# Kernel optimization log

Hardware: AMD Instinct MI355X
Metric: run time of the kernel (lower is better)

## Reference

```python
import jax, jax.numpy as jnp
import numpy as np

N_NODES = 100000
N_EDGES = 1600000
IN_CH = 64
HID = 64
OUT_CH = 16
T = 1.0


def _gat_layer(x, edge_index, W, b, t):
    # x: [N, d_in]; W: [d_out, d_in] (torch Linear weight layout); b: [d_out]
    N = x.shape[0]
    loop = jnp.arange(N, dtype=edge_index.dtype)
    src = jnp.concatenate([edge_index[0], loop])  # add self loops
    dst = jnp.concatenate([edge_index[1], loop])
    h = x @ W.T  # [N, d_out]
    x_i = h[dst]  # target node features per edge
    x_j = h[src]  # source node features per edge
    alpha = jnp.sum(x_i * x_j, axis=-1)  # [E']
    alpha = jnp.where(alpha > 0, jnp.asarray(t, h.dtype), jnp.asarray(-t, h.dtype))
    # segment softmax grouped by edge_index[0] (source), faithful to original
    m = jax.ops.segment_max(alpha, src, num_segments=N)
    e = jnp.exp(alpha - m[src])
    s = jax.ops.segment_sum(e, src, num_segments=N)
    w = e / s[src]
    msg = x_j * w[:, None]
    out = jax.ops.segment_sum(msg, dst, num_segments=N)  # scatter-add to target
    return out + b


def setup_inputs() -> dict:
    key = jax.random.key(0)
    k1, k2, k3, k4 = jax.random.split(key, 4)
    x = jax.random.normal(k1, (N_NODES, IN_CH), dtype=jnp.float32)
    edge_index = jax.random.randint(k2, (2, N_EDGES), 0, N_NODES, dtype=jnp.int64)
    # xavier-uniform-ish linear weights, torch layout [out, in]
    lim1 = float(np.sqrt(6.0 / (IN_CH + HID)))
    W1 = jax.random.uniform(k3, (HID, IN_CH), jnp.float32, -lim1, lim1)
    lim2 = float(np.sqrt(6.0 / (HID + OUT_CH)))
    W2 = jax.random.uniform(k4, (OUT_CH, HID), jnp.float32, -lim2, lim2)
    b1 = jnp.zeros((HID,), jnp.float32)
    b2 = jnp.zeros((OUT_CH,), jnp.float32)
    return {"x": x, "edge_index": edge_index, "W1": W1, "b1": b1, "W2": W2, "b2": b2}


def reference(x, edge_index, W1, b1, W2, b2):
    h = _gat_layer(x, edge_index, W1, b1, T)
    h = jax.nn.relu(h)
    h = _gat_layer(h, edge_index, W2, b2, T)
    return jax.nn.log_softmax(h, axis=1)
```

## Files before the change

kernel.cpp:

```cpp
#include <hip/hip_runtime.h>

#define EXPC 0.13533528323661270f
#define REP 8
#define CHUNK 16384

__global__ void zero_i32(int* __restrict__ p, int n) {
  int i = blockIdx.x * blockDim.x + threadIdx.x;
  if (i < n) p[i] = 0;
}

template <bool RELU_IN>
__global__ void __launch_bounds__(256, 1)
gemm64_k(const float* __restrict__ x, const float* __restrict__ W,
         float* __restrict__ h, int N) {
  __shared__ float xs[64][68];
  __shared__ float wt[64][68];
  const int t = threadIdx.x;
  const int r0 = blockIdx.x * 64;
  for (int i = t; i < 4096; i += 256) {
    int c = i >> 6, k = i & 63;
    wt[k][c] = W[i];
  }
  for (int s = t; s < 1024; s += 256) {
    int r = s >> 4, c4 = (s & 15) << 2;
    float4 v = make_float4(0.f, 0.f, 0.f, 0.f);
    if (r0 + r < N) {
      v = *(const float4*)(x + (size_t)(r0 + r) * 64 + c4);
      if (RELU_IN) {
        v.x = fmaxf(v.x, 0.f); v.y = fmaxf(v.y, 0.f);
        v.z = fmaxf(v.z, 0.f); v.w = fmaxf(v.w, 0.f);
      }
    }
    *(float4*)(&xs[r][c4]) = v;
  }
  __syncthreads();
  const int ty = t >> 4, tx = t & 15;
  float acc[4][4] = {};
  for (int kk = 0; kk < 64; kk += 4) {
    float4 a[4], w[4];
#pragma unroll
    for (int i = 0; i < 4; i++) a[i] = *(const float4*)(&xs[4 * ty + i][kk]);
#pragma unroll
    for (int m = 0; m < 4; m++) w[m] = *(const float4*)(&wt[kk + m][4 * tx]);
#pragma unroll
    for (int i = 0; i < 4; i++) {
      acc[i][0] = fmaf(a[i].x, w[0].x, fmaf(a[i].y, w[1].x,
                  fmaf(a[i].z, w[2].x, fmaf(a[i].w, w[3].x, acc[i][0]))));
      acc[i][1] = fmaf(a[i].x, w[0].y, fmaf(a[i].y, w[1].y,
                  fmaf(a[i].z, w[2].y, fmaf(a[i].w, w[3].y, acc[i][1]))));
      acc[i][2] = fmaf(a[i].x, w[0].z, fmaf(a[i].y, w[1].z,
                  fmaf(a[i].z, w[2].z, fmaf(a[i].w, w[3].z, acc[i][2]))));
      acc[i][3] = fmaf(a[i].x, w[0].w, fmaf(a[i].y, w[1].w,
                  fmaf(a[i].z, w[2].w, fmaf(a[i].w, w[3].w, acc[i][3]))));
    }
  }
#pragma unroll
  for (int i = 0; i < 4; i++) {
    int row = r0 + 4 * ty + i;
    if (row < N)
      *(float4*)(h + (size_t)row * 64 + 4 * tx) =
          make_float4(acc[i][0], acc[i][1], acc[i][2], acc[i][3]);
  }
}

__global__ void passA_k(const int* __restrict__ ei, int* __restrict__ chd,
                        int* __restrict__ chs, int E, int Et) {
  __shared__ int ld[512], ls[512];
  int t = threadIdx.x;
  for (int i = t; i < 512; i += 256) { ld[i] = 0; ls[i] = 0; }
  __syncthreads();
  int base = blockIdx.x * CHUNK;
  int end = base + CHUNK; if (end > Et) end = Et;
  for (int e = base + t; e < end; e += 256) {
    int s, d;
    if (e < E) { s = ei[e]; d = ei[E + e]; } else { s = e - E; d = s; }
    atomicAdd(&ld[d >> 8], 1);
    atomicAdd(&ls[s >> 8], 1);
  }
  __syncthreads();
  for (int i = t; i < 512; i += 256) {
    if (ld[i]) atomicAdd(chd + i, ld[i]);
    if (ls[i]) atomicAdd(chs + i, ls[i]);
  }
}

__global__ void scan2_k(const int* __restrict__ chd, const int* __restrict__ chs,
                        int* __restrict__ cbd, int* __restrict__ cbs,
                        int* __restrict__ cud, int* __restrict__ cus, int NB) {
  __shared__ int l[512];
  int t = threadIdx.x;
  for (int pass = 0; pass < 2; ++pass) {
    const int* src = pass ? chs : chd;
    int* db = pass ? cbs : cbd;
    int* dc = pass ? cus : cud;
    int v = (t < NB) ? src[t] : 0;
    l[t] = v;
    __syncthreads();
    for (int o = 1; o < 512; o <<= 1) {
      int a = (t >= o) ? l[t - o] : 0;
      __syncthreads();
      l[t] += a;
      __syncthreads();
    }
    if (t < NB) { int e = l[t] - v; db[t] = e; dc[t] = e; }
    __syncthreads();
  }
}

__global__ void passB_k(const int* __restrict__ ei, int* __restrict__ cud,
                        int* __restrict__ cus, int* __restrict__ part_dst,
                        unsigned char* __restrict__ part_src, int E, int Et) {
  __shared__ int cntd[512], cnts[512], based[512], bases[512];
  int t = threadIdx.x;
  for (int i = t; i < 512; i += 256) { cntd[i] = 0; cnts[i] = 0; }
  __syncthreads();
  int base = blockIdx.x * CHUNK;
  int end = base + CHUNK; if (end > Et) end = Et;
  for (int e = base + t; e < end; e += 256) {
    int s, d;
    if (e < E) { s = ei[e]; d = ei[E + e]; } else { s = e - E; d = s; }
    atomicAdd(&cntd[d >> 8], 1);
    atomicAdd(&cnts[s >> 8], 1);
  }
  __syncthreads();
  for (int i = t; i < 512; i += 256) {
    based[i] = cntd[i] ? atomicAdd(cud + i, cntd[i]) : 0;
    bases[i] = cnts[i] ? atomicAdd(cus + i, cnts[i]) : 0;
    cntd[i] = 0; cnts[i] = 0;
  }
  __syncthreads();
  for (int e = base + t; e < end; e += 256) {
    int s, d;
    if (e < E) { s = ei[e]; d = ei[E + e]; } else { s = e - E; d = s; }
    int bd = d >> 8, bs = s >> 8;
    int rd = atomicAdd(&cntd[bd], 1);
    int rs = atomicAdd(&cnts[bs], 1);
    part_dst[based[bd] + rd] = s | ((d & 255) << 17);
    part_src[bases[bs] + rs] = (unsigned char)(s & 255);
  }
}

__global__ void passC_k(const int* __restrict__ part_dst, const int* __restrict__ cbd,
                        const int* __restrict__ chd, int* __restrict__ csr_src,
                        int* __restrict__ in_deg, int* __restrict__ off, int N) {
  __shared__ int hist[256], loff[256], rank[256];
  int b = blockIdx.x, t = threadIdx.x;
  int segbase = cbd[b], segcnt = chd[b];
  hist[t] = 0; rank[t] = 0;
  __syncthreads();
  for (int i = t; i < segcnt; i += 256)
    atomicAdd(&hist[part_dst[segbase + i] >> 17], 1);
  __syncthreads();
  int x = hist[t];
  loff[t] = x;
  __syncthreads();
  for (int o = 1; o < 256; o <<= 1) {
    int a = (t >= o) ? loff[t - o] : 0;
    __syncthreads();
    loff[t] += a;
    __syncthreads();
  }
  int excl = loff[t] - x;
  int node = (b << 8) + t;
  if (node < N) { in_deg[node] = x; off[node] = segbase + excl; }
  __syncthreads();
  loff[t] = excl;
  __syncthreads();
  for (int i = t; i < segcnt; i += 256) {
    int rec = part_dst[segbase + i];
    int dl = rec >> 17;
    int r = atomicAdd(&rank[dl], 1);
    csr_src[segbase + loff[dl] + r] = rec & 0x1FFFF;
  }
}

__global__ void passCs_k(const unsigned char* __restrict__ part_src,
                         const int* __restrict__ cbs, const int* __restrict__ chs,
                         int* __restrict__ deg, int N) {
  __shared__ int hist[256];
  int b = blockIdx.x, t = threadIdx.x;
  int segbase = cbs[b], segcnt = chs[b];
  hist[t] = 0;
  __syncthreads();
  for (int i = t; i < segcnt; i += 256)
    atomicAdd(&hist[part_src[segbase + i]], 1);
  __syncthreads();
  int node = (b << 8) + t;
  if (node < N) deg[node] = hist[t];
}

template <int D>
__global__ void __launch_bounds__(256, 1)
alpha_csr_k(const int* __restrict__ csr_src, const int* __restrict__ off,
            const int* __restrict__ indeg, const float* __restrict__ h,
            unsigned char* __restrict__ flagb, int* __restrict__ pos_rep, int N) {
  const int G = D / 4;
  int t = blockIdx.x * 256 + threadIdx.x;
  int node = t / G;
  int c = t & (G - 1);
  if (node >= N) return;
  int* pos = pos_rep + (blockIdx.x & (REP - 1)) * N;
  const float4 hd = *(const float4*)(h + (size_t)node * D + c * 4);
  int j = off[node];
  int je = j + indeg[node];
  for (; j + 8 <= je; j += 8) {
    int s[8];
    float4 a[8];
#pragma unroll
    for (int u = 0; u < 8; u++) s[u] = csr_src[j + u];
#pragma unroll
    for (int u = 0; u < 8; u++) a[u] = *(const float4*)(h + (size_t)s[u] * D + c * 4);
    float p[8];
#pragma unroll
    for (int u = 0; u < 8; u++)
      p[u] = fmaf(a[u].x, hd.x, fmaf(a[u].y, hd.y, fmaf(a[u].z, hd.z, a[u].w * hd.w)));
#pragma unroll
    for (int o = G / 2; o > 0; o >>= 1) {
#pragma unroll
      for (int u = 0; u < 8; u++) p[u] += __shfl_xor(p[u], o);
    }
    if (c == 0) {
#pragma unroll
      for (int u = 0; u < 8; u++) {
        bool z = p[u] > 0.f;
        flagb[j + u] = (unsigned char)z;
        if (z) atomicAdd(pos + s[u], 1);
      }
    }
  }
  for (; j < je; ++j) {
    int s = csr_src[j];
    float4 hs = *(const float4*)(h + (size_t)s * D + c * 4);
    float p = fmaf(hs.x, hd.x, fmaf(hs.y, hd.y, fmaf(hs.z, hd.z, hs.w * hd.w)));
#pragma unroll
    for (int o = G / 2; o > 0; o >>= 1) p += __shfl_xor(p, o);
    if (c == 0) {
      bool pz = p > 0.f;
      flagb[j] = (unsigned char)pz;
      if (pz) atomicAdd(pos + s, 1);
    }
  }
}

template <int D>
__global__ void denom_scale_k(const int* __restrict__ pos_rep, const int* __restrict__ deg,
                              float* __restrict__ h, int N) {
  const int G = D / 4;
  int t = blockIdx.x * 256 + threadIdx.x;
  int node = t / G;
  int c = t & (G - 1);
  if (node >= N) return;
  float dinv = 0.f;
  if (c == 0) {
    int p = 0;
#pragma unroll
    for (int r = 0; r < REP; r++) p += pos_rep[r * N + node];
    int dg = deg[node];
    dinv = (p > 0) ? 1.f / ((float)p + (float)(dg - p) * EXPC)
                   : 1.f / (EXPC * (float)dg);
  }
  dinv = __shfl(dinv, 0, G);
  float4* hp = (float4*)(h + (size_t)node * D + c * 4);
  float4 v = *hp;
  v.x *= dinv; v.y *= dinv; v.z *= dinv; v.w *= dinv;
  *hp = v;
}

__global__ void __launch_bounds__(256, 1)
gather1_g16_k(const int* __restrict__ csr_src, const int* __restrict__ off,
              const int* __restrict__ indeg, const unsigned char* __restrict__ flagb,
              const float* __restrict__ h, const float* __restrict__ b1,
              const float* __restrict__ W2, float* __restrict__ h2, int N) {
  __shared__ float wt2[16][68];
  const int t = threadIdx.x;
  for (int i = t; i < 1024; i += 256) wt2[i >> 6][i & 63] = W2[i];
  __syncthreads();
  int g = blockIdx.x * 256 + t;
  int node = g >> 4;
  int c = g & 15;
  if (node >= N) return;
  float4 acc = *(const float4*)(b1 + c * 4);
  int j = off[node];
  int je = j + indeg[node];
  for (; j + 8 <= je; j += 8) {
    int s[8];
    float w[8];
    float4 v[8];
#pragma unroll
    for (int u = 0; u < 8; u++) s[u] = csr_src[j + u];
#pragma unroll
    for (int u = 0; u < 8; u++) w[u] = flagb[j + u] ? 1.f : EXPC;
#pragma unroll
    for (int u = 0; u < 8; u++) v[u] = *(const float4*)(h + (size_t)s[u] * 64 + c * 4);
#pragma unroll
    for (int u = 0; u < 8; u++) {
      acc.x = fmaf(w[u], v[u].x, acc.x);
      acc.y = fmaf(w[u], v[u].y, acc.y);
      acc.z = fmaf(w[u], v[u].z, acc.z);
      acc.w = fmaf(w[u], v[u].w, acc.w);
    }
  }
  for (; j < je; ++j) {
    int s = csr_src[j];
    float w = flagb[j] ? 1.f : EXPC;
    float4 hv = *(const float4*)(h + (size_t)s * 64 + c * 4);
    acc.x = fmaf(w, hv.x, acc.x);
    acc.y = fmaf(w, hv.y, acc.y);
    acc.z = fmaf(w, hv.z, acc.z);
    acc.w = fmaf(w, hv.w, acc.w);
  }
  acc.x = fmaxf(acc.x, 0.f); acc.y = fmaxf(acc.y, 0.f);
  acc.z = fmaxf(acc.z, 0.f); acc.w = fmaxf(acc.w, 0.f);
  int lanebase = (threadIdx.x & 63) & 48;
  float o = 0.f;
#pragma unroll
  for (int s16 = 0; s16 < 16; s16++) {
    int src = lanebase + s16;
    float cx = __shfl(acc.x, src);
    float cy = __shfl(acc.y, src);
    float cz = __shfl(acc.z, src);
    float cw = __shfl(acc.w, src);
    float4 wv = *(const float4*)(&wt2[c][4 * s16]);
    o = fmaf(cx, wv.x, fmaf(cy, wv.y, fmaf(cz, wv.z, fmaf(cw, wv.w, o))));
  }
  h2[(size_t)node * 16 + c] = o;
}

__global__ void __launch_bounds__(256, 1)
gather2_k(const int* __restrict__ csr_src, const int* __restrict__ off,
          const int* __restrict__ indeg, const unsigned char* __restrict__ flagb,
          const float* __restrict__ h, const float* __restrict__ b2,
          float* __restrict__ outp, int N) {
  int t = blockIdx.x * 256 + threadIdx.x;
  int node = t >> 2;
  int c = t & 3;
  if (node >= N) return;
  float4 acc = *(const float4*)(b2 + c * 4);
  int j = off[node];
  int je = j + indeg[node];
  for (; j + 8 <= je; j += 8) {
    int s[8];
    float w[8];
    float4 v[8];
#pragma unroll
    for (int u = 0; u < 8; u++) s[u] = csr_src[j + u];
#pragma unroll
    for (int u = 0; u < 8; u++) w[u] = flagb[j + u] ? 1.f : EXPC;
#pragma unroll
    for (int u = 0; u < 8; u++) v[u] = *(const float4*)(h + (size_t)s[u] * 16 + c * 4);
#pragma unroll
    for (int u = 0; u < 8; u++) {
      acc.x = fmaf(w[u], v[u].x, acc.x);
      acc.y = fmaf(w[u], v[u].y, acc.y);
      acc.z = fmaf(w[u], v[u].z, acc.z);
      acc.w = fmaf(w[u], v[u].w, acc.w);
    }
  }
  for (; j < je; ++j) {
    int s = csr_src[j];
    float w = flagb[j] ? 1.f : EXPC;
    float4 hv = *(const float4*)(h + (size_t)s * 16 + c * 4);
    acc.x = fmaf(w, hv.x, acc.x);
    acc.y = fmaf(w, hv.y, acc.y);
    acc.z = fmaf(w, hv.z, acc.z);
    acc.w = fmaf(w, hv.w, acc.w);
  }
  float m = fmaxf(fmaxf(acc.x, acc.y), fmaxf(acc.z, acc.w));
  m = fmaxf(m, __shfl_xor(m, 1));
  m = fmaxf(m, __shfl_xor(m, 2));
  float s = expf(acc.x - m) + expf(acc.y - m) + expf(acc.z - m) + expf(acc.w - m);
  s += __shfl_xor(s, 1);
  s += __shfl_xor(s, 2);
  float lse = m + logf(s);
  acc.x -= lse; acc.y -= lse; acc.z -= lse; acc.w -= lse;
  *(float4*)(outp + (size_t)node * 16 + c * 4) = acc;
}

extern "C" void kernel_launch(void* const* d_in, const int* in_sizes, int n_in,
                              void* d_out, int out_size, void* d_ws, size_t ws_size,
                              hipStream_t stream) {
  const float* x = (const float*)d_in[0];
  const int* ei = (const int*)d_in[1];
  const float* W1 = (const float*)d_in[2];
  const float* b1 = (const float*)d_in[3];
  const float* W2 = (const float*)d_in[4];
  const float* b2 = (const float*)d_in[5];
  float* out = (float*)d_out;

  const int N = in_sizes[0] / 64;
  const int E = in_sizes[1] / 2;
  const int Et = E + N;
  const int B = 256;
  const int nbT = (N + 63) / 64;
  const int NB = (N + 255) >> 8;
  const int nbP = (Et + CHUNK - 1) / CHUNK;

  char* ws = (char*)d_ws;
  float* h1 = (float*)ws;    ws += (size_t)N * 64 * 4;
  float* h2 = (float*)ws;    ws += (size_t)N * 16 * 4;
  int* deg = (int*)ws;       ws += (size_t)N * 4;
  int* in_deg = (int*)ws;    ws += (size_t)N * 4;
  int* off = (int*)ws;       ws += (size_t)N * 4;
  int* chd = (int*)ws;       ws += 512 * 4;
  int* chs = (int*)ws;       ws += 512 * 4;
  int* cbd = (int*)ws;       ws += 512 * 4;
  int* cbs = (int*)ws;       ws += 512 * 4;
  int* cud = (int*)ws;       ws += 512 * 4;
  int* cus = (int*)ws;       ws += 512 * 4;
  int* csr_src = (int*)ws;   ws += (size_t)Et * 4;
  char* P = ws;              ws += (size_t)Et * 4 + (size_t)Et;
  int* part_dst = (int*)P;
  unsigned char* part_src = (unsigned char*)(P + (size_t)Et * 4);
  int* pos_rep = (int*)P;
  unsigned char* flagb = (unsigned char*)(P + (size_t)REP * N * 4);

  hipLaunchKernelGGL(zero_i32, dim3(4), dim3(B), 0, stream, chd, 1024);
  hipLaunchKernelGGL(passA_k, dim3(nbP), dim3(B), 0, stream, ei, chd, chs, E, Et);
  hipLaunchKernelGGL(scan2_k, dim3(1), dim3(512), 0, stream, chd, chs, cbd, cbs, cud, cus, NB);
  hipLaunchKernelGGL(passB_k, dim3(nbP), dim3(B), 0, stream, ei, cud, cus,
                     part_dst, part_src, E, Et);
  hipLaunchKernelGGL(passC_k, dim3(NB), dim3(B), 0, stream, part_dst, cbd, chd,
                     csr_src, in_deg, off, N);
  hipLaunchKernelGGL(passCs_k, dim3(NB), dim3(B), 0, stream, part_src, cbs, chs, deg, N);

  hipLaunchKernelGGL((gemm64_k<false>), dim3(nbT), dim3(B), 0, stream, x, W1, h1, N);
  hipLaunchKernelGGL(zero_i32, dim3((REP * N + B - 1) / B), dim3(B), 0, stream,
                     pos_rep, REP * N);
  hipLaunchKernelGGL((alpha_csr_k<64>), dim3(((size_t)N * 16 + B - 1) / B), dim3(B), 0,
                     stream, csr_src, off, in_deg, h1, flagb, pos_rep, N);
  hipLaunchKernelGGL((denom_scale_k<64>), dim3(((size_t)N * 16 + B - 1) / B), dim3(B), 0,
                     stream, pos_rep, deg, h1, N);
  hipLaunchKernelGGL(gather1_g16_k, dim3(((size_t)N * 16 + B - 1) / B), dim3(B), 0,
                     stream, csr_src, off, in_deg, flagb, h1, b1, W2, h2, N);

  hipLaunchKernelGGL(zero_i32, dim3((REP * N + B - 1) / B), dim3(B), 0, stream,
                     pos_rep, REP * N);
  hipLaunchKernelGGL((alpha_csr_k<16>), dim3(((size_t)N * 4 + B - 1) / B), dim3(B), 0,
                     stream, csr_src, off, in_deg, h2, flagb, pos_rep, N);
  hipLaunchKernelGGL((denom_scale_k<16>), dim3(((size_t)N * 4 + B - 1) / B), dim3(B), 0,
                     stream, pos_rep, deg, h2, N);
  hipLaunchKernelGGL(gather2_k, dim3(((size_t)N * 4 + B - 1) / B), dim3(B), 0,
                     stream, csr_src, off, in_deg, flagb, h2, b2, out, N);
}
```

Measured before the change: 490.0 us.

## Use fp16 feature copies for attention sign test with exact fp32 fixup

```diff
diff --git a/kernel.cpp b/kernel.cpp
--- a/kernel.cpp
+++ b/kernel.cpp
@@ -1,18 +1,31 @@
 #include <hip/hip_runtime.h>
+#include <hip/hip_fp16.h>
 
 #define EXPC 0.13533528323661270f
 #define REP 8
 #define CHUNK 16384
+#define QREP 64
+#define QSLICE 8192
+#define BND 0.00390625f
+
+__device__ __forceinline__ float h2f_lo(unsigned u) {
+  return __half2float(__ushort_as_half((unsigned short)(u & 0xffffu)));
+}
+__device__ __forceinline__ float h2f_hi(unsigned u) {
+  return __half2float(__ushort_as_half((unsigned short)(u >> 16)));
+}
+__device__ __forceinline__ unsigned short f2h(float f) {
+  return __half_as_ushort(__float2half_rn(f));
+}
 
 __global__ void zero_i32(int* __restrict__ p, int n) {
   int i = blockIdx.x * blockDim.x + threadIdx.x;
   if (i < n) p[i] = 0;
 }
 
-template <bool RELU_IN>
 __global__ void __launch_bounds__(256, 1)
 gemm64_k(const float* __restrict__ x, const float* __restrict__ W,
-         float* __restrict__ h, int N) {
+         float* __restrict__ h, unsigned short* __restrict__ hh, int N) {
   __shared__ float xs[64][68];
   __shared__ float wt[64][68];
   const int t = threadIdx.x;
@@ -24,13 +37,7 @@
   for (int s = t; s < 1024; s += 256) {
     int r = s >> 4, c4 = (s & 15) << 2;
     float4 v = make_float4(0.f, 0.f, 0.f, 0.f);
-    if (r0 + r < N) {
-      v = *(const float4*)(x + (size_t)(r0 + r) * 64 + c4);
-      if (RELU_IN) {
-        v.x = fmaxf(v.x, 0.f); v.y = fmaxf(v.y, 0.f);
-        v.z = fmaxf(v.z, 0.f); v.w = fmaxf(v.w, 0.f);
-      }
-    }
+    if (r0 + r < N) v = *(const float4*)(x + (size_t)(r0 + r) * 64 + c4);
     *(float4*)(&xs[r][c4]) = v;
   }
   __syncthreads();
@@ -57,9 +64,13 @@
 #pragma unroll
   for (int i = 0; i < 4; i++) {
     int row = r0 + 4 * ty + i;
-    if (row < N)
+    if (row < N) {
       *(float4*)(h + (size_t)row * 64 + 4 * tx) =
           make_float4(acc[i][0], acc[i][1], acc[i][2], acc[i][3]);
+      unsigned p0 = (unsigned)f2h(acc[i][0]) | ((unsigned)f2h(acc[i][1]) << 16);
+      unsigned p1 = (unsigned)f2h(acc[i][2]) | ((unsigned)f2h(acc[i][3]) << 16);
+      *(uint2*)(hh + (size_t)row * 64 + 4 * tx) = make_uint2(p0, p1);
+    }
   }
 }
 
@@ -191,53 +202,111 @@
 
 template <int D>
 __global__ void __launch_bounds__(256, 1)
-alpha_csr_k(const int* __restrict__ csr_src, const int* __restrict__ off,
-            const int* __restrict__ indeg, const float* __restrict__ h,
-            unsigned char* __restrict__ flagb, int* __restrict__ pos_rep, int N) {
+alpha_h_k(const int* __restrict__ csr_src, const int* __restrict__ off,
+          const int* __restrict__ indeg, const unsigned short* __restrict__ hh,
+          unsigned char* __restrict__ flagb, int* __restrict__ pos_rep,
+          int2* __restrict__ q, int* __restrict__ qcnt, int N) {
   const int G = D / 4;
   int t = blockIdx.x * 256 + threadIdx.x;
   int node = t / G;
   int c = t & (G - 1);
   if (node >= N) return;
   int* pos = pos_rep + (blockIdx.x & (REP - 1)) * N;
-  const float4 hd = *(const float4*)(h + (size_t)node * D + c * 4);
-  int j = off[node];
-  int je = j + indeg[node];
+  int* qc = qcnt + (blockIdx.x & (QREP - 1));
+  int2* qs = q + (size_t)(blockIdx.x & (QREP - 1)) * QSLICE;
+  uint2 rd = *(const uint2*)(hh + (size_t)node * D + c * 4);
+  float d0 = h2f_lo(rd.x), d1 = h2f_hi(rd.x), d2 = h2f_lo(rd.y), d3 = h2f_hi(rd.y);
+  float b0 = fabsf(d0), b1 = fabsf(d1), b2 = fabsf(d2), b3 = fabsf(d3);
+  int j = off[node], je = j + indeg[node];
   for (; j + 8 <= je; j += 8) {
     int s[8];
-    float4 a[8];
+    uint2 r[8];
 #pragma unroll
     for (int u = 0; u < 8; u++) s[u] = csr_src[j + u];
 #pragma unroll
-    for (int u = 0; u < 8; u++) a[u] = *(const float4*)(h + (size_t)s[u] * D + c * 4);
-    float p[8];
-#pragma unroll
-    for (int u = 0; u < 8; u++)
-      p[u] = fmaf(a[u].x, hd.x, fmaf(a[u].y, hd.y, fmaf(a[u].z, hd.z, a[u].w * hd.w)));
+    for (int u = 0; u < 8; u++) r[u] = *(const uint2*)(hh + (size_t)s[u] * D + c * 4);
+    float p[8], qv[8];
+#pragma unroll
+    for (int u = 0; u < 8; u++) {
+      float x0 = h2f_lo(r[u].x), x1 = h2f_hi(r[u].x);
+      float x2 = h2f_lo(r[u].y), x3 = h2f_hi(r[u].y);
+      p[u] = fmaf(x0, d0, fmaf(x1, d1, fmaf(x2, d2, x3 * d3)));
+      qv[u] = fmaf(fabsf(x0), b0, fmaf(fabsf(x1), b1, fmaf(fabsf(x2), b2, fabsf(x3) * b3)));
+    }
 #pragma unroll
     for (int o = G / 2; o > 0; o >>= 1) {
 #pragma unroll
-      for (int u = 0; u < 8; u++) p[u] += __shfl_xor(p[u], o);
+      for (int u = 0; u < 8; u++) { p[u] += __shfl_xor(p[u], o); qv[u] += __shfl_xor(qv[u], o); }
     }
     if (c == 0) {
 #pragma unroll
       for (int u = 0; u < 8; u++) {
-        bool z = p[u] > 0.f;
-        flagb[j + u] = (unsigned char)z;
-        if (z) atomicAdd(pos + s[u], 1);
+        if (fabsf(p[u]) > qv[u] * BND) {
+          bool z = p[u] > 0.f;
+          flagb[j + u] = (unsigned char)z;
+          if (z) atomicAdd(pos + s[u], 1);
+        } else {
+          int qi = atomicAdd(qc, 1);
+          if (qi < QSLICE) qs[qi] = make_int2(j + u, node);
+          else {
+            bool z = p[u] > 0.f;
+            flagb[j + u] = (unsigned char)z;
+            if (z) atomicAdd(pos + s[u], 1);
+          }
+        }
       }
     }
   }
   for (; j < je; ++j) {
     int s = csr_src[j];
-    float4 hs = *(const float4*)(h + (size_t)s * D + c * 4);
-    float p = fmaf(hs.x, hd.x, fmaf(hs.y, hd.y, fmaf(hs.z, hd.z, hs.w * hd.w)));
+    uint2 r = *(const uint2*)(hh + (size_t)s * D + c * 4);
+    float x0 = h2f_lo(r.x), x1 = h2f_hi(r.x), x2 = h2f_lo(r.y), x3 = h2f_hi(r.y);
+    float p = fmaf(x0, d0, fmaf(x1, d1, fmaf(x2, d2, x3 * d3)));
+    float qv = fmaf(fabsf(x0), b0, fmaf(fabsf(x1), b1, fmaf(fabsf(x2), b2, fabsf(x3) * b3)));
+#pragma unroll
+    for (int o = G / 2; o > 0; o >>= 1) { p += __shfl_xor(p, o); qv += __shfl_xor(qv, o); }
+    if (c == 0) {
+      if (fabsf(p) > qv * BND) {
+        bool z = p > 0.f;
+        flagb[j] = (unsigned char)z;
+        if (z) atomicAdd(pos + s, 1);
+      } else {
+        int qi = atomicAdd(qc, 1);
+        if (qi < QSLICE) qs[qi] = make_int2(j, node);
+        else {
+          bool z = p > 0.f;
+          flagb[j] = (unsigned char)z;
+          if (z) atomicAdd(pos + s, 1);
+        }
+      }
+    }
+  }
+}
+
+template <int D>
+__global__ void fixup_k(const int2* __restrict__ q, const int* __restrict__ qcnt,
+                        const int* __restrict__ csr_src, const float* __restrict__ h,
+                        unsigned char* __restrict__ flagb, int* __restrict__ pos_rep, int N) {
+  const int G = D / 4;
+  int slice = blockIdx.x & (QREP - 1);
+  int n = qcnt[slice]; if (n > QSLICE) n = QSLICE;
+  const int2* qs = q + (size_t)slice * QSLICE;
+  int* pos = pos_rep + (blockIdx.x & (REP - 1)) * N;
+  int gid = ((blockIdx.x >> 6) * 256 + threadIdx.x) / G;
+  int c = threadIdx.x & (G - 1);
+  int stride = (gridDim.x >> 6) * (256 / G);
+  for (int i = gid; i < n; i += stride) {
+    int j = qs[i].x, d = qs[i].y;
+    int s = csr_src[j];
+    const float4 av = *(const float4*)(h + (size_t)s * D + c * 4);
+    const float4 dv = *(const float4*)(h + (size_t)d * D + c * 4);
+    float p = fmaf(av.x, dv.x, fmaf(av.y, dv.y, fmaf(av.z, dv.z, av.w * dv.w)));
 #pragma unroll
     for (int o = G / 2; o > 0; o >>= 1) p += __shfl_xor(p, o);
     if (c == 0) {
-      bool pz = p > 0.f;
-      flagb[j] = (unsigned char)pz;
-      if (pz) atomicAdd(pos + s, 1);
+      bool z = p > 0.f;
+      flagb[j] = (unsigned char)z;
+      if (z) atomicAdd(pos + s, 1);
     }
   }
 }
@@ -266,11 +335,37 @@
   *hp = v;
 }
 
+template <int D>
+__global__ void denom_scale_h_k(const int* __restrict__ pos_rep, const int* __restrict__ deg,
+                                const float* __restrict__ h, unsigned short* __restrict__ hh,
+                                int N) {
+  const int G = D / 4;
+  int t = blockIdx.x * 256 + threadIdx.x;
+  int node = t / G;
+  int c = t & (G - 1);
+  if (node >= N) return;
+  float dinv = 0.f;
+  if (c == 0) {
+    int p = 0;
+#pragma unroll
+    for (int r = 0; r < REP; r++) p += pos_rep[r * N + node];
+    int dg = deg[node];
+    dinv = (p > 0) ? 1.f / ((float)p + (float)(dg - p) * EXPC)
+                   : 1.f / (EXPC * (float)dg);
+  }
+  dinv = __shfl(dinv, 0, G);
+  const float4 v = *(const float4*)(h + (size_t)node * D + c * 4);
+  unsigned p0 = (unsigned)f2h(v.x * dinv) | ((unsigned)f2h(v.y * dinv) << 16);
+  unsigned p1 = (unsigned)f2h(v.z * dinv) | ((unsigned)f2h(v.w * dinv) << 16);
+  *(uint2*)(hh + (size_t)node * D + c * 4) = make_uint2(p0, p1);
+}
+
 __global__ void __launch_bounds__(256, 1)
 gather1_g16_k(const int* __restrict__ csr_src, const int* __restrict__ off,
               const int* __restrict__ indeg, const unsigned char* __restrict__ flagb,
               const float* __restrict__ h, const float* __restrict__ b1,
-              const float* __restrict__ W2, float* __restrict__ h2, int N) {
+              const float* __restrict__ W2, float* __restrict__ h2,
+              unsigned short* __restrict__ h2h, int N) {
   __shared__ float wt2[16][68];
   const int t = threadIdx.x;
   for (int i = t; i < 1024; i += 256) wt2[i >> 6][i & 63] = W2[i];
@@ -324,12 +419,13 @@
     o = fmaf(cx, wv.x, fmaf(cy, wv.y, fmaf(cz, wv.z, fmaf(cw, wv.w, o))));
   }
   h2[(size_t)node * 16 + c] = o;
+  h2h[(size_t)node * 16 + c] = f2h(o);
 }
 
 __global__ void __launch_bounds__(256, 1)
 gather2_k(const int* __restrict__ csr_src, const int* __restrict__ off,
           const int* __restrict__ indeg, const unsigned char* __restrict__ flagb,
-          const float* __restrict__ h, const float* __restrict__ b2,
+          const unsigned short* __restrict__ hh, const float* __restrict__ b2,
           float* __restrict__ outp, int N) {
   int t = blockIdx.x * 256 + threadIdx.x;
   int node = t >> 2;
@@ -341,29 +437,29 @@
   for (; j + 8 <= je; j += 8) {
     int s[8];
     float w[8];
-    float4 v[8];
+    uint2 r[8];
 #pragma unroll
     for (int u = 0; u < 8; u++) s[u] = csr_src[j + u];
 #pragma unroll
     for (int u = 0; u < 8; u++) w[u] = flagb[j + u] ? 1.f : EXPC;
 #pragma unroll
-    for (int u = 0; u < 8; u++) v[u] = *(const float4*)(h + (size_t)s[u] * 16 + c * 4);
+    for (int u = 0; u < 8; u++) r[u] = *(const uint2*)(hh + (size_t)s[u] * 16 + c * 4);
 #pragma unroll
     for (int u = 0; u < 8; u++) {
-      acc.x = fmaf(w[u], v[u].x, acc.x);
-      acc.y = fmaf(w[u], v[u].y, acc.y);
-      acc.z = fmaf(w[u], v[u].z, acc.z);
-      acc.w = fmaf(w[u], v[u].w, acc.w);
+      acc.x = fmaf(w[u], h2f_lo(r[u].x), acc.x);
+      acc.y = fmaf(w[u], h2f_hi(r[u].x), acc.y);
+      acc.z = fmaf(w[u], h2f_lo(r[u].y), acc.z);
+      acc.w = fmaf(w[u], h2f_hi(r[u].y), acc.w);
     }
   }
   for (; j < je; ++j) {
     int s = csr_src[j];
     float w = flagb[j] ? 1.f : EXPC;
-    float4 hv = *(const float4*)(h + (size_t)s * 16 + c * 4);
-    acc.x = fmaf(w, hv.x, acc.x);
-    acc.y = fmaf(w, hv.y, acc.y);
-    acc.z = fmaf(w, hv.z, acc.z);
-    acc.w = fmaf(w, hv.w, acc.w);
+    uint2 r = *(const uint2*)(hh + (size_t)s * 16 + c * 4);
+    acc.x = fmaf(w, h2f_lo(r.x), acc.x);
+    acc.y = fmaf(w, h2f_hi(r.x), acc.y);
+    acc.z = fmaf(w, h2f_lo(r.y), acc.z);
+    acc.w = fmaf(w, h2f_hi(r.y), acc.w);
   }
   float m = fmaxf(fmaxf(acc.x, acc.y), fmaxf(acc.z, acc.w));
   m = fmaxf(m, __shfl_xor(m, 1));
@@ -396,23 +492,27 @@
   const int nbP = (Et + CHUNK - 1) / CHUNK;
 
   char* ws = (char*)d_ws;
-  float* h1 = (float*)ws;    ws += (size_t)N * 64 * 4;
-  float* h2 = (float*)ws;    ws += (size_t)N * 16 * 4;
-  int* deg = (int*)ws;       ws += (size_t)N * 4;
-  int* in_deg = (int*)ws;    ws += (size_t)N * 4;
-  int* off = (int*)ws;       ws += (size_t)N * 4;
-  int* chd = (int*)ws;       ws += 512 * 4;
-  int* chs = (int*)ws;       ws += 512 * 4;
-  int* cbd = (int*)ws;       ws += 512 * 4;
-  int* cbs = (int*)ws;       ws += 512 * 4;
-  int* cud = (int*)ws;       ws += 512 * 4;
-  int* cus = (int*)ws;       ws += 512 * 4;
-  int* csr_src = (int*)ws;   ws += (size_t)Et * 4;
-  char* P = ws;              ws += (size_t)Et * 4 + (size_t)Et;
+  float* h1 = (float*)ws;            ws += (size_t)N * 64 * 4;
+  unsigned short* h1h = (unsigned short*)ws; ws += (size_t)N * 64 * 2;
+  float* h2 = (float*)ws;            ws += (size_t)N * 16 * 4;
+  unsigned short* h2h = (unsigned short*)ws; ws += (size_t)N * 16 * 2;
+  int* deg = (int*)ws;               ws += (size_t)N * 4;
+  int* in_deg = (int*)ws;            ws += (size_t)N * 4;
+  int* off = (int*)ws;               ws += (size_t)N * 4;
+  int* chd = (int*)ws;               ws += 512 * 4;
+  int* chs = (int*)ws;               ws += 512 * 4;
+  int* cbd = (int*)ws;               ws += 512 * 4;
+  int* cbs = (int*)ws;               ws += 512 * 4;
+  int* cud = (int*)ws;               ws += 512 * 4;
+  int* cus = (int*)ws;               ws += 512 * 4;
+  int* csr_src = (int*)ws;           ws += (size_t)Et * 4;
+  int2* qbuf = (int2*)ws;            ws += (size_t)QREP * QSLICE * 8;
+  char* P = ws;                      ws += (size_t)Et * 4 + (size_t)Et;
   int* part_dst = (int*)P;
   unsigned char* part_src = (unsigned char*)(P + (size_t)Et * 4);
   int* pos_rep = (int*)P;
-  unsigned char* flagb = (unsigned char*)(P + (size_t)REP * N * 4);
+  int* qcnt = (int*)(P + (size_t)REP * N * 4);
+  unsigned char* flagb = (unsigned char*)(P + (size_t)REP * N * 4 + 256);
 
   hipLaunchKernelGGL(zero_i32, dim3(4), dim3(B), 0, stream, chd, 1024);
   hipLaunchKernelGGL(passA_k, dim3(nbP), dim3(B), 0, stream, ei, chd, chs, E, Et);
@@ -423,22 +523,26 @@
                      csr_src, in_deg, off, N);
   hipLaunchKernelGGL(passCs_k, dim3(NB), dim3(B), 0, stream, part_src, cbs, chs, deg, N);
 
-  hipLaunchKernelGGL((gemm64_k<false>), dim3(nbT), dim3(B), 0, stream, x, W1, h1, N);
-  hipLaunchKernelGGL(zero_i32, dim3((REP * N + B - 1) / B), dim3(B), 0, stream,
-                     pos_rep, REP * N);
-  hipLaunchKernelGGL((alpha_csr_k<64>), dim3(((size_t)N * 16 + B - 1) / B), dim3(B), 0,
-                     stream, csr_src, off, in_deg, h1, flagb, pos_rep, N);
+  hipLaunchKernelGGL(gemm64_k, dim3(nbT), dim3(B), 0, stream, x, W1, h1, h1h, N);
+  hipLaunchKernelGGL(zero_i32, dim3((REP * N + QREP + B - 1) / B), dim3(B), 0, stream,
+                     pos_rep, REP * N + QREP);
+  hipLaunchKernelGGL((alpha_h_k<64>), dim3(((size_t)N * 16 + B - 1) / B), dim3(B), 0,
+                     stream, csr_src, off, in_deg, h1h, flagb, pos_rep, qbuf, qcnt, N);
+  hipLaunchKernelGGL((fixup_k<64>), dim3(1024), dim3(B), 0, stream,
+                     qbuf, qcnt, csr_src, h1, flagb, pos_rep, N);
   hipLaunchKernelGGL((denom_scale_k<64>), dim3(((size_t)N * 16 + B - 1) / B), dim3(B), 0,
                      stream, pos_rep, deg, h1, N);
   hipLaunchKernelGGL(gather1_g16_k, dim3(((size_t)N * 16 + B - 1) / B), dim3(B), 0,
-                     stream, csr_src, off, in_deg, flagb, h1, b1, W2, h2, N);
-
-  hipLaunchKernelGGL(zero_i32, dim3((REP * N + B - 1) / B), dim3(B), 0, stream,
-                     pos_rep, REP * N);
-  hipLaunchKernelGGL((alpha_csr_k<16>), dim3(((size_t)N * 4 + B - 1) / B), dim3(B), 0,
-                     stream, csr_src, off, in_deg, h2, flagb, pos_rep, N);
-  hipLaunchKernelGGL((denom_scale_k<16>), dim3(((size_t)N * 4 + B - 1) / B), dim3(B), 0,
-                     stream, pos_rep, deg, h2, N);
+                     stream, csr_src, off, in_deg, flagb, h1, b1, W2, h2, h2h, N);
+
+  hipLaunchKernelGGL(zero_i32, dim3((REP * N + QREP + B - 1) / B), dim3(B), 0, stream,
+                     pos_rep, REP * N + QREP);
+  hipLaunchKernelGGL((alpha_h_k<16>), dim3(((size_t)N * 4 + B - 1) / B), dim3(B), 0,
+                     stream, csr_src, off, in_deg, h2h, flagb, pos_rep, qbuf, qcnt, N);
+  hipLaunchKernelGGL((fixup_k<16>), dim3(1024), dim3(B), 0, stream,
+                     qbuf, qcnt, csr_src, h2, flagb, pos_rep, N);
+  hipLaunchKernelGGL((denom_scale_h_k<16>), dim3(((size_t)N * 4 + B - 1) / B), dim3(B), 0,
+                     stream, pos_rep, deg, h2, h2h, N);
   hipLaunchKernelGGL(gather2_k, dim3(((size_t)N * 4 + B - 1) / B), dim3(B), 0,
-                     stream, csr_src, off, in_deg, flagb, h2, b2, out, N);
-}
+                     stream, csr_src, off, in_deg, flagb, h2h, b2, out, N);
+}
```

New measurement: 587.4 us. 19.9% more time.
